# Kernel tuning notes

Hardware: AMD Instinct MI355X
Metric: run time of the kernel (lower is better)

Reference implementation:

```python
import jax, jax.numpy as jnp
import numpy as np
from jax import lax

F = 8  # db4 filter length
_DEC_LO = np.array([-0.010597401784997278, 0.032883011666982945,
                    0.030841381835986965, -0.18703481171888114,
                    -0.02798376941698385, 0.6308807679295904,
                    0.7148465705525415, 0.23037781330885523], dtype=np.float32)
_DEC_HI = np.array([(-1.0) ** (k + 1) * _DEC_LO[k] for k in range(F)], dtype=np.float32)
_REC_LO = _DEC_LO[::-1].copy()
_REC_HI = _DEC_HI[::-1].copy()
# lax.conv is cross-correlation; flip filters to get np.convolve semantics.
DEC_KERN = jnp.asarray(np.stack([_DEC_LO[::-1], _DEC_HI[::-1]])[:, None, :])   # [2,1,F]
REC_KERN = jnp.asarray(np.stack([_REC_LO[::-1], _REC_HI[::-1]])[None, :, :])   # [1,2,F]
REC_LO_KERN = jnp.asarray(_REC_LO[::-1][None, None, :])                        # [1,1,F]


def dwt1(x):
    """Single-level db4 DWT, pywt/ptwt 'reflect' mode. x:[N,L] -> (lp,hp) each [N, floor((L+F-1)/2)]."""
    xp = jnp.pad(x, ((0, 0), (F - 1, F - 1)), mode='reflect')[:, 1:]
    y = lax.conv_general_dilated(xp[:, None, :], DEC_KERN,
                                 window_strides=(2,), padding='VALID')
    return y[:, 0], y[:, 1]


def idwt(ca, cd, out_len):
    """Single-level inverse db4 DWT (pywt waverec step): out_len = 2*C - F + 2."""
    u = jnp.stack([ca, cd], axis=1)  # [N,2,C]
    y = lax.conv_general_dilated(u, REC_KERN, window_strides=(1,),
                                 padding=[(F - 1, F - 1)], lhs_dilation=(2,))
    return y[:, 0, F - 2:F - 2 + out_len]


def idwt_lo(ca, out_len):
    """Inverse DWT with zero detail coefficients (baseline upsampling)."""
    y = lax.conv_general_dilated(ca[:, None, :], REC_LO_KERN, window_strides=(1,),
                                 padding=[(F - 1, F - 1)], lhs_dilation=(2,))
    return y[:, 0, F - 2:F - 2 + out_len]


def calculate_baseline(s):
    """s:[N,L]. Iterative lowpass pyramid with per-row SSD local-minimum stopping rule.
    The torch version shrinks the active row set; here we keep the full batch and track a
    per-row stop depth, which provably yields identical results (depths are set at most once,
    and the torch data-dependent 'all stopped' break only skips unused computation)."""
    N = s.shape[0]
    sigs = [s]
    ssds = []
    depth = jnp.full((N,), -1, dtype=jnp.int32)
    t = 0
    while True:  # static unroll: bounded by (lp length < 8) or (iter > 7)
        lp, hp = dwt1(sigs[t])
        ssds.append(jnp.sum(hp * hp, axis=-1))
        if t >= 2:
            newly = (ssds[t - 2] > ssds[t - 1]) & (ssds[t - 1] < ssds[t]) & (depth < 0)
            depth = jnp.where(newly, t, depth)
            if lp.shape[-1] < 8 or t > 7:
                break
        sigs.append(lp)
        t += 1
    depth = jnp.where(depth < 0, t, depth)  # rows never stopped keep the deepest level
    bl = sigs[-1]
    for k in range(len(sigs) - 2, -1, -1):
        rec = idwt_lo(bl, sigs[k].shape[-1])  # waverec([lp, zeros]) + odd-length trim
        bl = jnp.where((depth >= k + 1)[:, None], rec, sigs[k])
    return bl


def f_remove_baseline(x):
    s = x.reshape(-1, x.shape[-1])
    bl = calculate_baseline(s).reshape(x.shape)
    return x - lax.stop_gradient(bl)  # torch detaches the baseline


def f_remove_hf_noise(x):
    s = x.reshape(-1, x.shape[-1])
    ca, details = s, []
    for _ in range(4):  # level = 4
        ca, cd = dwt1(ca)
        details.append(cd)  # [cD1, cD2, cD3, cD4]
    flat = jnp.sort(jnp.abs(details[-1]).ravel())
    sigma = flat[(flat.shape[0] - 1) // 2] / jnp.float32(0.6745)  # torch.median = lower middle
    details = [jnp.where(d < sigma, jnp.float32(0), d) for d in details]  # signed threshold, as in source
    for cd in reversed(details):
        if ca.shape[-1] == cd.shape[-1] + 1:
            ca = ca[:, :-1]
        ca = idwt(ca, cd, 2 * cd.shape[-1] - F + 2)
    return ca.reshape(x.shape)


def f_normalize(x):
    mean = jnp.mean(x, axis=-1, keepdims=True)
    std = jnp.std(x, axis=-1, keepdims=True, ddof=1)  # torch.std_mean is unbiased
    return jnp.nan_to_num((x - mean) / std)


def setup_inputs() -> dict:
    key = jax.random.key(0)
    x = jax.random.normal(key, (512, 12, 5000), dtype=jnp.float32)
    return {"x": x}


def reference(x):
    x = f_remove_baseline(x)
    x = f_remove_hf_noise(x)
    x = f_normalize(x)  # result_only=True: std/mean aux outputs are discarded
    return x
```

## Files before the change

### kernel.cpp

```cpp
#include <hip/hip_runtime.h>
#include <math.h>

#define NROWS 6144
#define LSIG  5000
#define NT    256

#define DL0 (-0.010597401784997278f)
#define DL1 ( 0.032883011666982945f)
#define DL2 ( 0.030841381835986965f)
#define DL3 (-0.18703481171888114f)
#define DL4 (-0.02798376941698385f)
#define DL5 ( 0.6308807679295904f)
#define DL6 ( 0.7148465705525415f)
#define DL7 ( 0.23037781330885523f)
#define DH0 ( 0.010597401784997278f)
#define DH1 ( 0.032883011666982945f)
#define DH2 (-0.030841381835986965f)
#define DH3 (-0.18703481171888114f)
#define DH4 ( 0.02798376941698385f)
#define DH5 ( 0.6308807679295904f)
#define DH6 (-0.7148465705525415f)
#define DH7 ( 0.23037781330885523f)

__device__ __forceinline__ void dwt_pair_edge(const float* __restrict__ src, int L, int k,
                                              float& a, float& b) {
    const float LO[8] = {DL0,DL1,DL2,DL3,DL4,DL5,DL6,DL7};
    const float HI[8] = {DH0,DH1,DH2,DH3,DH4,DH5,DH6,DH7};
    a = 0.f; b = 0.f;
    int base = 2*k - 6;
#pragma unroll
    for (int t = 0; t < 8; ++t) {
        int j = base + t;
        int i = (j < 0) ? -j : j;
        if (i >= L) i = 2*L - 2 - i;
        float v = src[i];
        a += v * LO[7-t];
        b += v * HI[7-t];
    }
}

__device__ __forceinline__ void dwt_pair_int(const float* __restrict__ src, int k,
                                             float& a, float& b) {
    int base = 2*k - 6;
    float v0 = src[base],     v1 = src[base + 1], v2 = src[base + 2], v3 = src[base + 3];
    float v4 = src[base + 4], v5 = src[base + 5], v6 = src[base + 6], v7 = src[base + 7];
    a = v0*DL7 + v1*DL6 + v2*DL5 + v3*DL4 + v4*DL3 + v5*DL2 + v6*DL1 + v7*DL0;
    b = v0*DH7 + v1*DH6 + v2*DH5 + v3*DH4 + v4*DH3 + v5*DH2 + v6*DH1 + v7*DH0;
}

__device__ __forceinline__ void idwt_lo_pair(const float* __restrict__ ca, int m,
                                             float& ev, float& od) {
    float c0 = ca[m], c1 = ca[m+1], c2 = ca[m+2], c3 = ca[m+3];
    ev = c0*DL1 + c1*DL3 + c2*DL5 + c3*DL7;
    od = c0*DL0 + c1*DL2 + c2*DL4 + c3*DL6;
}

__device__ __forceinline__ void idwt_pair(const float* __restrict__ ca, const float* __restrict__ cd,
                                          int m, float& ev, float& od) {
    float c0 = ca[m], c1 = ca[m+1], c2 = ca[m+2], c3 = ca[m+3];
    float e0 = cd[m], e1 = cd[m+1], e2 = cd[m+2], e3 = cd[m+3];
    ev = c0*DL1 + c1*DL3 + c2*DL5 + c3*DL7 + e0*DH1 + e1*DH3 + e2*DH5 + e3*DH7;
    od = c0*DL0 + c1*DL2 + c2*DL4 + c3*DL6 + e0*DH0 + e1*DH2 + e2*DH4 + e3*DH6;
}

__global__ __launch_bounds__(NT, 4) void kernelA(const float* __restrict__ x,
                                                 float* __restrict__ g_d1, float* __restrict__ g_d2,
                                                 float* __restrict__ g_d3, float* __restrict__ g_d4,
                                                 float* __restrict__ g_ca4) {
    __shared__ float sig0[5000];
    __shared__ float pyr[5028];
    __shared__ float redm[9][4];
    __shared__ int depth_s;

    const int row = blockIdx.x;
    const int tid = threadIdx.x;

    {
        const float4* xr4 = (const float4*)(x + (size_t)row * LSIG);
        float4* s4 = (float4*)sig0;
        for (int i = tid; i < 1250; i += NT) s4[i] = xr4[i];
    }
    __syncthreads();

    const int lensA[10] = {5000, 2503, 1255, 631, 319, 163, 85, 46, 26, 16};
    const int offs[8]   = {0, 2503, 3758, 4389, 4708, 4871, 4956, 5002};

    float sp[9];
    const float* src = sig0;
#pragma unroll
    for (int t = 0; t < 9; ++t) {
        const int L   = lensA[t];
        const int Lo  = lensA[t + 1];
        const int kHi = (L - 2) >> 1;
        float* lp = pyr + ((t < 8) ? offs[t] : 0);
        float part = 0.f;
        for (int k = tid; k < Lo; k += NT) {
            float a, b;
            if (k >= 3 && k <= kHi) dwt_pair_int(src, k, a, b);
            else                    dwt_pair_edge(src, L, k, a, b);
            if (t < 8) lp[k] = a;
            part += b * b;
        }
        sp[t] = part;
        __syncthreads();
        src = lp;
    }

#pragma unroll
    for (int t = 0; t < 9; ++t) {
        float p = sp[t];
#pragma unroll
        for (int o = 32; o; o >>= 1) p += __shfl_down(p, o, 64);
        if ((tid & 63) == 0) redm[t][tid >> 6] = p;
    }
    __syncthreads();
    if (tid == 0) {
        float ssds[9];
#pragma unroll
        for (int t = 0; t < 9; ++t) ssds[t] = redm[t][0] + redm[t][1] + redm[t][2] + redm[t][3];
        int dd = -1;
        for (int t = 2; t <= 8; ++t)
            if (dd < 0 && ssds[t - 2] > ssds[t - 1] && ssds[t - 1] < ssds[t]) dd = t;
        depth_s = (dd < 0) ? 8 : dd;
    }
    __syncthreads();
    const int d = depth_s;

    const float* cur = pyr + offs[d - 1];
    for (int k = d - 1; k >= 1; --k) {
        const int ol = lensA[k];
        float* dst = (k & 1) ? pyr : (pyr + 2503);
        const int np = (ol + 1) >> 1;
        for (int m = tid; m < np; m += NT) {
            float ev, od;
            idwt_lo_pair(cur, m, ev, od);
            dst[2*m] = ev;
            if (2*m + 1 < ol) dst[2*m + 1] = od;
        }
        __syncthreads();
        cur = dst;
    }
    for (int m = tid; m < 2500; m += NT) {
        float ev, od;
        idwt_lo_pair(cur, m, ev, od);
        sig0[2*m]     -= ev;
        sig0[2*m + 1] -= od;
    }
    __syncthreads();

    const int l2[5] = {5000, 2503, 1255, 631, 319};
    src = sig0;
#pragma unroll
    for (int lev = 0; lev < 4; ++lev) {
        const int L   = l2[lev];
        const int Lo  = l2[lev + 1];
        const int kHi = (L - 2) >> 1;
        float* lp = pyr + ((lev & 1) ? 2503 : 0);
        float* hg;
        if      (lev == 0) hg = g_d1 + (size_t)row * 2503;
        else if (lev == 1) hg = g_d2 + (size_t)row * 1255;
        else if (lev == 2) hg = g_d3 + (size_t)row * 631;
        else               hg = g_d4 + (size_t)row * 319;
        for (int k = tid; k < Lo; k += NT) {
            float a, b;
            if (k >= 3 && k <= kHi) dwt_pair_int(src, k, a, b);
            else                    dwt_pair_edge(src, L, k, a, b);
            lp[k] = a;
            hg[k] = b;
        }
        __syncthreads();
        src = lp;
    }
    float* cg = g_ca4 + (size_t)row * 319;
    for (int i = tid; i < 319; i += NT) cg[i] = pyr[2503 + i];
}

__global__ void kinit(unsigned* bins, unsigned* state) {
    int i = blockIdx.x * blockDim.x + threadIdx.x;
    if (i < 2048) bins[i] = 0u;
    if (i == 0) { state[0] = 0u; state[1] = 979967u; }
}

__global__ void khist(const float* __restrict__ data, int n, unsigned* __restrict__ bins,
                      const unsigned* __restrict__ state, int shift, unsigned binmask,
                      unsigned prefmask) {
    __shared__ unsigned h[2048];
    const int nb = (int)binmask + 1;
    for (int i = threadIdx.x; i < nb; i += blockDim.x) h[i] = 0u;
    __syncthreads();
    const unsigned pref = state[0] & prefmask;
    const int stride = gridDim.x * blockDim.x;
    for (int i = blockIdx.x * blockDim.x + threadIdx.x; i < n; i += stride) {
        unsigned key = __float_as_uint(fabsf(data[i]));
        if ((key & prefmask) == pref) atomicAdd(&h[(key >> shift) & binmask], 1u);
    }
    __syncthreads();
    for (int i = threadIdx.x; i < nb; i += blockDim.x)
        if (h[i]) atomicAdd(&bins[i], h[i]);
}

__global__ void kselect(unsigned* bins, unsigned* state, float* sigma_out,
                        int shift, int nbins, int final_pass) {
    if (threadIdx.x == 0) {
        unsigned krem = state[1];
        unsigned prefix = state[0];
        unsigned cum = 0;
        int b = 0;
        for (; b < nbins - 1; ++b) {
            unsigned c = bins[b];
            if (cum + c > krem) break;
            cum += c;
        }
        prefix |= ((unsigned)b) << shift;
        state[0] = prefix;
        state[1] = krem - cum;
        if (final_pass) *sigma_out = __uint_as_float(prefix) / 0.6745f;
    }
    __syncthreads();
    for (int i = threadIdx.x; i < nbins; i += blockDim.x) bins[i] = 0u;
}

__global__ __launch_bounds__(NT, 4) void kernelC(const float* __restrict__ g_d1,
                                                 const float* __restrict__ g_d2,
                                                 const float* __restrict__ g_d3,
                                                 const float* __restrict__ g_d4,
                                                 const float* __restrict__ g_ca4,
                                                 const float* __restrict__ sigma_p,
                                                 float* __restrict__ out) {
    __shared__ float A[5000];
    __shared__ float B[2504];
    __shared__ float Dd[2503];
    __shared__ double redd[4][2];
    __shared__ float sg;

    const int row = blockIdx.x;
    const int tid = threadIdx.x;
    if (tid == 0) sg = *sigma_p;
    for (int i = tid; i < 319; i += NT) A[i] = g_ca4[(size_t)row * 319 + i];
    __syncthreads();
    const float sigma = sg;

    const int Cs[4] = {319, 631, 1255, 2503};
    const int Os[4] = {632, 1256, 2504, 5000};

#pragma unroll
    for (int s = 0; s < 4; ++s) {
        const int C = Cs[s];
        const int O = Os[s];
        const float* dg;
        if      (s == 0) dg = g_d4 + (size_t)row * 319;
        else if (s == 1) dg = g_d3 + (size_t)row * 631;
        else if (s == 2) dg = g_d2 + (size_t)row * 1255;
        else             dg = g_d1 + (size_t)row * 2503;
        const float* spb = (s & 1) ? B : A;
        float* dp        = (s & 1) ? A : B;
        for (int i = tid; i < C; i += NT) {
            float v = dg[i];
            Dd[i] = (v < sigma) ? 0.f : v;
        }
        __syncthreads();
        const int np = O >> 1;
        for (int m = tid; m < np; m += NT) {
            float ev, od;
            idwt_pair(spb, Dd, m, ev, od);
            dp[2*m]     = ev;
            dp[2*m + 1] = od;
        }
        __syncthreads();
    }

    double s1 = 0.0, s2 = 0.0;
    for (int i = tid; i < 5000; i += NT) {
        double v = (double)A[i];
        s1 += v;
        s2 += v * v;
    }
#pragma unroll
    for (int o = 32; o; o >>= 1) {
        s1 += __shfl_down(s1, o, 64);
        s2 += __shfl_down(s2, o, 64);
    }
    if ((tid & 63) == 0) { redd[tid >> 6][0] = s1; redd[tid >> 6][1] = s2; }
    __syncthreads();
    double sum  = redd[0][0] + redd[1][0] + redd[2][0] + redd[3][0];
    double sumq = redd[0][1] + redd[1][1] + redd[2][1] + redd[3][1];
    double mean = sum / 5000.0;
    double var  = (sumq - sum * mean) / 4999.0;

    float meanf = (float)mean;
    float inv = 1.0f / (float)sqrt(var);
    float* orow = out + (size_t)row * 5000;
    for (int i = tid; i < 5000; i += NT) {
        float r = (A[i] - meanf) * inv;
        if (isnan(r)) r = 0.f;
        else if (isinf(r)) r = copysignf(3.4028234663852886e38f, r);
        orow[i] = r;
    }
}

extern "C" void kernel_launch(void* const* d_in, const int* in_sizes, int n_in,
                              void* d_out, int out_size, void* d_ws, size_t ws_size,
                              hipStream_t stream) {
    const float* x = (const float*)d_in[0];
    float* out = (float*)d_out;

    const size_t n1 = (size_t)NROWS * 2503;
    const size_t n2 = (size_t)NROWS * 1255;
    const size_t n3 = (size_t)NROWS * 631;
    const size_t n4 = (size_t)NROWS * 319;

    float* w    = (float*)d_ws;
    float* d1   = w;
    float* d2   = d1 + n1;
    float* d3   = d2 + n2;
    float* d4   = d3 + n3;
    float* ca4  = d4 + n4;
    unsigned* bins  = (unsigned*)(ca4 + n4);
    unsigned* state = bins + 2048;
    float* sigp = (float*)(state + 2);
    const int n = (int)n4;

    hipLaunchKernelGGL(kernelA, dim3(NROWS), dim3(NT), 0, stream, x, d1, d2, d3, d4, ca4);
    hipLaunchKernelGGL(kinit, dim3(8), dim3(256), 0, stream, bins, state);
    hipLaunchKernelGGL(khist, dim3(512), dim3(256), 0, stream, d4, n, bins, state, 21, 2047u, 0x00000000u);
    hipLaunchKernelGGL(kselect, dim3(1), dim3(256), 0, stream, bins, state, sigp, 21, 2048, 0);
    hipLaunchKernelGGL(khist, dim3(512), dim3(256), 0, stream, d4, n, bins, state, 10, 2047u, 0xFFE00000u);
    hipLaunchKernelGGL(kselect, dim3(1), dim3(256), 0, stream, bins, state, sigp, 10, 2048, 0);
    hipLaunchKernelGGL(khist, dim3(512), dim3(256), 0, stream, d4, n, bins, state, 0, 1023u, 0xFFFFFC00u);
    hipLaunchKernelGGL(kselect, dim3(1), dim3(256), 0, stream, bins, state, sigp, 0, 1024, 1);
    hipLaunchKernelGGL(kernelC, dim3(NROWS), dim3(NT), 0, stream, d1, d2, d3, d4, ca4, sigp, out);
}
```

Measured before the change: 497.1 us.

## Shrink LDS footprint, fuse median select into one cooperative kernel

Kernel A now uses a single 7503-float shared buffer with aliased pyramid offsets, and it rereads x from global memory for the baseline subtraction. This lowers LDS use so launch bounds can rise to 5 blocks per CU. The six histogram/select launches and the init kernel are replaced by one cooperative kernel that uses grid syncs and a wave-parallel prefix-scan select. Kernel C thresholds the detail coefficients while reading them from global memory instead of staging them in LDS, which drops one barrier per level. In exchange there are redundant global reads of the details, reliance on cooperative-launch residency, and the risk that the bins zeroed inside kernel A are not complete.

```diff
diff --git a/kernel.cpp b/kernel.cpp
--- a/kernel.cpp
+++ b/kernel.cpp
@@ -1,5 +1,8 @@
 #include <hip/hip_runtime.h>
+#include <hip/hip_cooperative_groups.h>
 #include <math.h>
+
+namespace cg = cooperative_groups;
 
 #define NROWS 6144
 #define LSIG  5000
@@ -55,44 +58,38 @@
     od = c0*DL0 + c1*DL2 + c2*DL4 + c3*DL6;
 }
 
-__device__ __forceinline__ void idwt_pair(const float* __restrict__ ca, const float* __restrict__ cd,
-                                          int m, float& ev, float& od) {
-    float c0 = ca[m], c1 = ca[m+1], c2 = ca[m+2], c3 = ca[m+3];
-    float e0 = cd[m], e1 = cd[m+1], e2 = cd[m+2], e3 = cd[m+3];
-    ev = c0*DL1 + c1*DL3 + c2*DL5 + c3*DL7 + e0*DH1 + e1*DH3 + e2*DH5 + e3*DH7;
-    od = c0*DL0 + c1*DL2 + c2*DL4 + c3*DL6 + e0*DH0 + e1*DH2 + e2*DH4 + e3*DH6;
-}
-
-__global__ __launch_bounds__(NT, 4) void kernelA(const float* __restrict__ x,
+__global__ __launch_bounds__(NT, 5) void kernelA(const float* __restrict__ x,
                                                  float* __restrict__ g_d1, float* __restrict__ g_d2,
                                                  float* __restrict__ g_d3, float* __restrict__ g_d4,
-                                                 float* __restrict__ g_ca4) {
-    __shared__ float sig0[5000];
-    __shared__ float pyr[5028];
+                                                 float* __restrict__ g_ca4,
+                                                 unsigned* __restrict__ bins_all) {
+    __shared__ float S[7503];
     __shared__ float redm[9][4];
     __shared__ int depth_s;
 
     const int row = blockIdx.x;
     const int tid = threadIdx.x;
 
+    if (blockIdx.x < 20) bins_all[blockIdx.x * NT + tid] = 0u;
+
     {
         const float4* xr4 = (const float4*)(x + (size_t)row * LSIG);
-        float4* s4 = (float4*)sig0;
+        float4* s4 = (float4*)S;
         for (int i = tid; i < 1250; i += NT) s4[i] = xr4[i];
     }
     __syncthreads();
 
-    const int lensA[10] = {5000, 2503, 1255, 631, 319, 163, 85, 46, 26, 16};
-    const int offs[8]   = {0, 2503, 3758, 4389, 4708, 4871, 4956, 5002};
+    const int lensA[10]    = {5000, 2503, 1255, 631, 319, 163, 85, 46, 26, 16};
+    const int sigs_off[9]  = {0, 5000, 0, 1255, 1886, 2205, 2368, 2453, 2499};
 
     float sp[9];
-    const float* src = sig0;
 #pragma unroll
     for (int t = 0; t < 9; ++t) {
         const int L   = lensA[t];
         const int Lo  = lensA[t + 1];
         const int kHi = (L - 2) >> 1;
-        float* lp = pyr + ((t < 8) ? offs[t] : 0);
+        const float* src = S + sigs_off[t];
+        float* lp = (t < 8) ? (S + sigs_off[t + 1]) : (float*)nullptr;
         float part = 0.f;
         for (int k = tid; k < Lo; k += NT) {
             float a, b;
@@ -103,7 +100,6 @@
         }
         sp[t] = part;
         __syncthreads();
-        src = lp;
     }
 
 #pragma unroll
@@ -126,10 +122,10 @@
     __syncthreads();
     const int d = depth_s;
 
-    const float* cur = pyr + offs[d - 1];
+    const float* cur = S + sigs_off[d];
     for (int k = d - 1; k >= 1; --k) {
         const int ol = lensA[k];
-        float* dst = (k & 1) ? pyr : (pyr + 2503);
+        float* dst = S + ((k & 1) ? 5000 : 2525);
         const int np = (ol + 1) >> 1;
         for (int m = tid; m < np; m += NT) {
             float ev, od;
@@ -140,87 +136,155 @@
         __syncthreads();
         cur = dst;
     }
-    for (int m = tid; m < 2500; m += NT) {
-        float ev, od;
-        idwt_lo_pair(cur, m, ev, od);
-        sig0[2*m]     -= ev;
-        sig0[2*m + 1] -= od;
+    {
+        const float2* x2 = (const float2*)(x + (size_t)row * LSIG);
+        for (int m = tid; m < 2500; m += NT) {
+            float ev, od;
+            idwt_lo_pair(cur, m, ev, od);
+            float2 xv = x2[m];
+            S[2*m]     = xv.x - ev;
+            S[2*m + 1] = xv.y - od;
+        }
     }
     __syncthreads();
 
     const int l2[5] = {5000, 2503, 1255, 631, 319};
-    src = sig0;
+    const int srcoff[4] = {0, 5000, 0, 1255};
+    const int dstoff[4] = {5000, 0, 1255, 0 };
 #pragma unroll
     for (int lev = 0; lev < 4; ++lev) {
         const int L   = l2[lev];
         const int Lo  = l2[lev + 1];
         const int kHi = (L - 2) >> 1;
-        float* lp = pyr + ((lev & 1) ? 2503 : 0);
+        const float* src = S + srcoff[lev];
+        float* lp = S + dstoff[lev];
         float* hg;
         if      (lev == 0) hg = g_d1 + (size_t)row * 2503;
         else if (lev == 1) hg = g_d2 + (size_t)row * 1255;
         else if (lev == 2) hg = g_d3 + (size_t)row * 631;
         else               hg = g_d4 + (size_t)row * 319;
+        float* cg = g_ca4 + (size_t)row * 319;
         for (int k = tid; k < Lo; k += NT) {
             float a, b;
             if (k >= 3 && k <= kHi) dwt_pair_int(src, k, a, b);
             else                    dwt_pair_edge(src, L, k, a, b);
-            lp[k] = a;
+            if (lev < 3) lp[k] = a;
+            else         cg[k] = a;
             hg[k] = b;
         }
         __syncthreads();
-        src = lp;
-    }
-    float* cg = g_ca4 + (size_t)row * 319;
-    for (int i = tid; i < 319; i += NT) cg[i] = pyr[2503 + i];
-}
-
-__global__ void kinit(unsigned* bins, unsigned* state) {
-    int i = blockIdx.x * blockDim.x + threadIdx.x;
-    if (i < 2048) bins[i] = 0u;
-    if (i == 0) { state[0] = 0u; state[1] = 979967u; }
-}
-
-__global__ void khist(const float* __restrict__ data, int n, unsigned* __restrict__ bins,
-                      const unsigned* __restrict__ state, int shift, unsigned binmask,
-                      unsigned prefmask) {
+    }
+}
+
+__device__ __forceinline__ void select_in_lds(unsigned* h, int nb, int shift,
+                                              unsigned prefix_in, unsigned krem_in,
+                                              unsigned* state, float* sigma_out,
+                                              int final_pass, int tid) {
+    if (tid < 64) {
+        const int sl = nb >> 6;
+        const int base = tid * sl;
+        unsigned s = 0;
+        for (int j = 0; j < sl; ++j) s += h[base + j];
+        unsigned c = s;
+#pragma unroll
+        for (int o = 1; o < 64; o <<= 1) {
+            unsigned t = __shfl_up(c, o, 64);
+            if (tid >= o) c += t;
+        }
+        unsigned long long m = __ballot(c > krem_in);
+        int tseg = __ffsll(m) - 1;
+        if (tid == tseg) {
+            unsigned cum = c - s;
+            int b = base;
+            for (int j = 0; j < sl; ++j) {
+                unsigned cc = h[base + j];
+                if (cum + cc > krem_in) { b = base + j; break; }
+                cum += cc;
+            }
+            unsigned pref = prefix_in | ((unsigned)b << shift);
+            __hip_atomic_store(&state[0], pref, __ATOMIC_RELEASE, __HIP_MEMORY_SCOPE_AGENT);
+            __hip_atomic_store(&state[1], krem_in - cum, __ATOMIC_RELEASE, __HIP_MEMORY_SCOPE_AGENT);
+            if (final_pass) *sigma_out = __uint_as_float(pref) / 0.6745f;
+        }
+    }
+}
+
+__global__ __launch_bounds__(NT) void kmedian(const float* __restrict__ d4, int n,
+                                              unsigned* __restrict__ bins0,
+                                              unsigned* __restrict__ bins1,
+                                              unsigned* __restrict__ bins2,
+                                              unsigned* __restrict__ state,
+                                              float* __restrict__ sigma_out) {
+    cg::grid_group grid = cg::this_grid();
     __shared__ unsigned h[2048];
-    const int nb = (int)binmask + 1;
-    for (int i = threadIdx.x; i < nb; i += blockDim.x) h[i] = 0u;
-    __syncthreads();
-    const unsigned pref = state[0] & prefmask;
-    const int stride = gridDim.x * blockDim.x;
-    for (int i = blockIdx.x * blockDim.x + threadIdx.x; i < n; i += stride) {
-        unsigned key = __float_as_uint(fabsf(data[i]));
-        if ((key & prefmask) == pref) atomicAdd(&h[(key >> shift) & binmask], 1u);
-    }
-    __syncthreads();
-    for (int i = threadIdx.x; i < nb; i += blockDim.x)
-        if (h[i]) atomicAdd(&bins[i], h[i]);
-}
-
-__global__ void kselect(unsigned* bins, unsigned* state, float* sigma_out,
-                        int shift, int nbins, int final_pass) {
-    if (threadIdx.x == 0) {
-        unsigned krem = state[1];
-        unsigned prefix = state[0];
-        unsigned cum = 0;
-        int b = 0;
-        for (; b < nbins - 1; ++b) {
-            unsigned c = bins[b];
-            if (cum + c > krem) break;
-            cum += c;
-        }
-        prefix |= ((unsigned)b) << shift;
-        state[0] = prefix;
-        state[1] = krem - cum;
-        if (final_pass) *sigma_out = __uint_as_float(prefix) / 0.6745f;
-    }
-    __syncthreads();
-    for (int i = threadIdx.x; i < nbins; i += blockDim.x) bins[i] = 0u;
-}
-
-__global__ __launch_bounds__(NT, 4) void kernelC(const float* __restrict__ g_d1,
+    const int tid = threadIdx.x;
+    const int gsz = (int)gridDim.x * NT;
+    const int gid = (int)blockIdx.x * NT + tid;
+
+    for (int i = tid; i < 2048; i += NT) h[i] = 0u;
+    __syncthreads();
+    for (int i = gid; i < n; i += gsz)
+        atomicAdd(&h[__float_as_uint(fabsf(d4[i])) >> 21], 1u);
+    __syncthreads();
+    for (int i = tid; i < 2048; i += NT) if (h[i]) atomicAdd(&bins0[i], h[i]);
+    grid.sync();
+    if (blockIdx.x == 0) {
+        for (int i = tid; i < 2048; i += NT) h[i] = bins0[i];
+        __syncthreads();
+        select_in_lds(h, 2048, 21, 0u, 979967u, state, sigma_out, 0, tid);
+    }
+    grid.sync();
+
+    unsigned pref = __hip_atomic_load(&state[0], __ATOMIC_ACQUIRE, __HIP_MEMORY_SCOPE_AGENT);
+    unsigned krem = __hip_atomic_load(&state[1], __ATOMIC_ACQUIRE, __HIP_MEMORY_SCOPE_AGENT);
+    for (int i = tid; i < 2048; i += NT) h[i] = 0u;
+    __syncthreads();
+    for (int i = gid; i < n; i += gsz) {
+        unsigned key = __float_as_uint(fabsf(d4[i]));
+        if ((key & 0xFFE00000u) == pref) atomicAdd(&h[(key >> 10) & 2047u], 1u);
+    }
+    __syncthreads();
+    for (int i = tid; i < 2048; i += NT) if (h[i]) atomicAdd(&bins1[i], h[i]);
+    grid.sync();
+    if (blockIdx.x == 0) {
+        for (int i = tid; i < 2048; i += NT) h[i] = bins1[i];
+        __syncthreads();
+        select_in_lds(h, 2048, 10, pref, krem, state, sigma_out, 0, tid);
+    }
+    grid.sync();
+
+    pref = __hip_atomic_load(&state[0], __ATOMIC_ACQUIRE, __HIP_MEMORY_SCOPE_AGENT);
+    krem = __hip_atomic_load(&state[1], __ATOMIC_ACQUIRE, __HIP_MEMORY_SCOPE_AGENT);
+    for (int i = tid; i < 1024; i += NT) h[i] = 0u;
+    __syncthreads();
+    for (int i = gid; i < n; i += gsz) {
+        unsigned key = __float_as_uint(fabsf(d4[i]));
+        if ((key & 0xFFFFFC00u) == pref) atomicAdd(&h[key & 1023u], 1u);
+    }
+    __syncthreads();
+    for (int i = tid; i < 1024; i += NT) if (h[i]) atomicAdd(&bins2[i], h[i]);
+    grid.sync();
+    if (blockIdx.x == 0) {
+        for (int i = tid; i < 1024; i += NT) h[i] = bins2[i];
+        __syncthreads();
+        select_in_lds(h, 1024, 0, pref, krem, state, sigma_out, 1, tid);
+    }
+}
+
+__device__ __forceinline__ void idwt_pair_g(const float* __restrict__ ca,
+                                            const float* __restrict__ dg, float sigma,
+                                            int m, float& ev, float& od) {
+    float c0 = ca[m], c1 = ca[m+1], c2 = ca[m+2], c3 = ca[m+3];
+    float e0 = dg[m],   e1 = dg[m+1], e2 = dg[m+2], e3 = dg[m+3];
+    e0 = (e0 < sigma) ? 0.f : e0;
+    e1 = (e1 < sigma) ? 0.f : e1;
+    e2 = (e2 < sigma) ? 0.f : e2;
+    e3 = (e3 < sigma) ? 0.f : e3;
+    ev = c0*DL1 + c1*DL3 + c2*DL5 + c3*DL7 + e0*DH1 + e1*DH3 + e2*DH5 + e3*DH7;
+    od = c0*DL0 + c1*DL2 + c2*DL4 + c3*DL6 + e0*DH0 + e1*DH2 + e2*DH4 + e3*DH6;
+}
+
+__global__ __launch_bounds__(NT, 5) void kernelC(const float* __restrict__ g_d1,
                                                  const float* __restrict__ g_d2,
                                                  const float* __restrict__ g_d3,
                                                  const float* __restrict__ g_d4,
@@ -229,7 +293,6 @@
                                                  float* __restrict__ out) {
     __shared__ float A[5000];
     __shared__ float B[2504];
-    __shared__ float Dd[2503];
     __shared__ double redd[4][2];
     __shared__ float sg;
 
@@ -254,15 +317,11 @@
         else             dg = g_d1 + (size_t)row * 2503;
         const float* spb = (s & 1) ? B : A;
         float* dp        = (s & 1) ? A : B;
-        for (int i = tid; i < C; i += NT) {
-            float v = dg[i];
-            Dd[i] = (v < sigma) ? 0.f : v;
-        }
-        __syncthreads();
         const int np = O >> 1;
+        (void)C;
         for (int m = tid; m < np; m += NT) {
             float ev, od;
-            idwt_pair(spb, Dd, m, ev, od);
+            idwt_pair_g(spb, dg, sigma, m, ev, od);
             dp[2*m]     = ev;
             dp[2*m + 1] = od;
         }
@@ -315,18 +374,23 @@
     float* d3   = d2 + n2;
     float* d4   = d3 + n3;
     float* ca4  = d4 + n4;
-    unsigned* bins  = (unsigned*)(ca4 + n4);
-    unsigned* state = bins + 2048;
+    unsigned* bins0 = (unsigned*)(ca4 + n4);
+    unsigned* bins1 = bins0 + 2048;
+    unsigned* bins2 = bins1 + 2048;
+    unsigned* state = bins2 + 1024;
     float* sigp = (float*)(state + 2);
-    const int n = (int)n4;
-
-    hipLaunchKernelGGL(kernelA, dim3(NROWS), dim3(NT), 0, stream, x, d1, d2, d3, d4, ca4);
-    hipLaunchKernelGGL(kinit, dim3(8), dim3(256), 0, stream, bins, state);
-    hipLaunchKernelGGL(khist, dim3(512), dim3(256), 0, stream, d4, n, bins, state, 21, 2047u, 0x00000000u);
-    hipLaunchKernelGGL(kselect, dim3(1), dim3(256), 0, stream, bins, state, sigp, 21, 2048, 0);
-    hipLaunchKernelGGL(khist, dim3(512), dim3(256), 0, stream, d4, n, bins, state, 10, 2047u, 0xFFE00000u);
-    hipLaunchKernelGGL(kselect, dim3(1), dim3(256), 0, stream, bins, state, sigp, 10, 2048, 0);
-    hipLaunchKernelGGL(khist, dim3(512), dim3(256), 0, stream, d4, n, bins, state, 0, 1023u, 0xFFFFFC00u);
-    hipLaunchKernelGGL(kselect, dim3(1), dim3(256), 0, stream, bins, state, sigp, 0, 1024, 1);
-    hipLaunchKernelGGL(kernelC, dim3(NROWS), dim3(NT), 0, stream, d1, d2, d3, d4, ca4, sigp, out);
-}
+    int n = (int)n4;
+
+    hipLaunchKernelGGL(kernelA, dim3(NROWS), dim3(NT), 0, stream,
+                       x, d1, d2, d3, d4, ca4, bins0);
+
+    {
+        const float* d4c = d4;
+        void* args[] = {(void*)&d4c, (void*)&n, (void*)&bins0, (void*)&bins1,
+                        (void*)&bins2, (void*)&state, (void*)&sigp};
+        hipLaunchCooperativeKernel((void*)kmedian, dim3(512), dim3(NT), args, 0, stream);
+    }
+
+    hipLaunchKernelGGL(kernelC, dim3(NROWS), dim3(NT), 0, stream,
+                       d1, d2, d3, d4, ca4, sigp, out);
+}
```

After: 709.2 us. 1.43x slower.
